# Kernel optimization log

Measured on AMD Instinct MI355X. Metric: run time of the kernel, lower is better.

Reference implementation:

```python
import jax, jax.numpy as jnp
import numpy as np

B, S, DM, H = 4, 1024, 1024, 16
DK = DM // H  # 64, must equal embeddim=64

def _linear(x, W, b):
    # torch nn.Linear: y = x @ W.T + b, W is [out, in]
    return jnp.matmul(x, W.T) + b

def setup_inputs() -> dict:
    key = jax.random.key(0)
    ks = jax.random.split(key, 40)
    inp = {}
    inp["query"] = jax.random.normal(ks[0], (B, S, DM), jnp.float32)
    inp["key"] = jax.random.normal(ks[1], (B, S, DM), jnp.float32)
    inp["value"] = jax.random.normal(ks[2], (B, S, DM), jnp.float32)
    inp["mask"] = jnp.ones((B, S, S), jnp.int32)
    def mk(i, dout, din):
        W = jax.random.normal(ks[i], (dout, din), jnp.float32) / np.sqrt(din).astype(np.float32)
        b = jax.random.normal(ks[i + 20], (dout,), jnp.float32) * 0.01
        return W, b
    # the 4 d_model x d_model projection linears (q, k, v, out)
    inp["Wq"], inp["bq"] = mk(3, DM, DM)
    inp["Wk"], inp["bk"] = mk(4, DM, DM)
    inp["Wv"], inp["bv"] = mk(5, DM, DM)
    inp["Wo"], inp["bo"] = mk(6, DM, DM)
    # the 64x64 refinement linears
    inp["Wkl"], inp["bkl"] = mk(7, DK, DK)   # key_linear
    inp["Wql"], inp["bql"] = mk(8, DK, DK)   # query_linear
    inp["Wq2"], inp["bq2"] = mk(9, DK, DK)   # query2_linear
    inp["Wvl"], inp["bvl"] = mk(10, DK, DK)  # value_linear
    inp["Wel"], inp["bel"] = mk(11, DK, DK)  # embed_linear
    return inp

def reference(query, key, value, mask,
              Wq, bq, Wk, bk, Wv, bv, Wo, bo,
              Wkl, bkl, Wql, bql, Wq2, bq2, Wvl, bvl, Wel, bel):
    b, s, dm = query.shape
    # project and split heads: [b, h, s, d_k]
    def split(x):
        return x.reshape(b, s, H, DK).transpose(0, 2, 1, 3)
    q = split(_linear(query, Wq, bq))
    k = split(_linear(key, Wk, bk))
    v = split(_linear(value, Wv, bv))
    # per-head 64x64 refinements with relu
    key_refine = jax.nn.relu(_linear(k, Wkl, bkl))
    q1 = jax.nn.relu(_linear(q, Wql, bql))
    q1 = jax.nn.relu(_linear(q1, Wel, bel))
    q2 = jax.nn.relu(_linear(q, Wq2, bq2))
    v_refine = jax.nn.relu(_linear(v, Wvl, bvl))
    # two attention-like matmuls (no 1/sqrt(d_k) scaling in original)
    qv = jnp.einsum("bhqd,bhkd->bhqk", q2, v_refine)
    kq = jnp.einsum("bhqd,bhkd->bhqk", q1, key_refine)
    m = mask[:, None, :, :]  # mask.unsqueeze(1)
    kq = jnp.where(m == 0, jnp.float32(-1e9), kq)
    attn = jax.nn.softmax(kq, axis=-1)
    # elementwise combine, then matmul against raw projected key (not value!)
    out = jnp.einsum("bhqk,bhkd->bhqd", attn * qv, k)
    out = out.transpose(0, 2, 1, 3).reshape(b, s, dm)
    return _linear(out, Wo, bo)
```

## Files before the change

kernel.cpp:

```cpp
#include <hip/hip_runtime.h>
#include <hip/hip_bf16.h>

#define B_  4
#define S_  1024
#define DM_ 1024
#define H_  16
#define DK_ 64

typedef unsigned short u16;
typedef __attribute__((ext_vector_type(8))) short bf16x8;
typedef __attribute__((ext_vector_type(4))) float f32x4;

__device__ __forceinline__ float bf2f(u16 u) {
    union { unsigned int i; float f; } c;
    c.i = ((unsigned int)u) << 16;
    return c.f;
}
__device__ __forceinline__ u16 f2bf(float f) {
    union { float f; unsigned int i; } c;
    c.f = f;
    unsigned int x = c.i;
    unsigned int lsb = (x >> 16) & 1u;
    x += 0x7fffu + lsb;
    return (u16)(x >> 16);
}
__device__ __forceinline__ u16 f2bf_fast(float f) {
    __hip_bfloat16 h = __float2bfloat16(f);
    return *reinterpret_cast<u16*>(&h);
}

__device__ __forceinline__ void async_ld16(const u16* g, u16* l) {
    __builtin_amdgcn_global_load_lds(
        (const __attribute__((address_space(1))) unsigned int*)(const void*)g,
        (__attribute__((address_space(3))) unsigned int*)(void*)l, 16, 0, 0);
}

__global__ void detect_kernel(const u16* __restrict__ q, int* __restrict__ flag) {
    int lane = threadIdx.x & 63;
    int cnt = 0;
#pragma unroll
    for (int i = 0; i < 4; ++i) {
        u16 u = q[2 * (lane * 4 + i)];
        int e = (u >> 7) & 0xFF;
        cnt += (e >= 100 && e <= 140) ? 1 : 0;
    }
#pragma unroll
    for (int off = 1; off < 64; off <<= 1) cnt += __shfl_xor(cnt, off, 64);
    if (lane == 0) *flag = (cnt < 128) ? 1 : 0;
}

#define NSEG 12
struct CvtArgs {
    const void* src[NSEG];
    void*       dst[NSEG];
    unsigned    off[NSEG + 1];
};

__global__ __launch_bounds__(256) void prep_kernel(
    CvtArgs a, unsigned total, const int* __restrict__ flag,
    const int* __restrict__ mask, int* __restrict__ tflags)
{
    const int tid = threadIdx.x;
    if (blockIdx.x < 512) {
        const int bx = blockIdx.x;
        const int kt = bx & 15, b = (bx >> 4) & 3, z = bx >> 6;
        int ok = 1;
#pragma unroll
        for (int i = tid; i < 128 * 16; i += 256) {
            int row = z * 128 + (i >> 4), seg = i & 15;
            int4 m = *(const int4*)&mask[((size_t)b * S_ + row) * S_ + kt * 64 + seg * 4];
            ok &= (m.x != 0) & (m.y != 0) & (m.z != 0) & (m.w != 0);
        }
        if (!ok) atomicOr(&tflags[b * 16 + kt], 1);
        return;
    }
    if (!*flag) return;
    unsigned v = (blockIdx.x - 512) * 256 + tid;
    if (v >= total) return;
    int s = 0;
    while (s < NSEG - 1 && v >= a.off[s + 1]) ++s;
    unsigned local = v - a.off[s];
    u16* dp = (u16*)a.dst[s] + (size_t)local * 8;
    const float* sp = (const float*)a.src[s] + (size_t)local * 8;
    float4 x = *(const float4*)sp, y = *(const float4*)(sp + 4);
    u16 t[8] = {f2bf(x.x), f2bf(x.y), f2bf(x.z), f2bf(x.w),
                f2bf(y.x), f2bf(y.y), f2bf(y.z), f2bf(y.w)};
    *(uint4*)dp = *(uint4*)t;
}

__global__ __launch_bounds__(256) void transpose_kernel(
    const u16* __restrict__ kp, u16* __restrict__ kpt)
{
    __shared__ u16 T[64][65];
    const int s0 = blockIdx.x * 64, h = blockIdx.y, b = blockIdx.z;
    const int tid = threadIdx.x;
    const size_t base = (size_t)b * S_ * DM_ + (size_t)h * DK_;
    for (int c = tid; c < 512; c += 256) {
        int row = c >> 3, cc = (c & 7) * 8;
        union { uint4 v; u16 u[8]; } x;
        x.v = *(const uint4*)&kp[base + (size_t)(s0 + row) * DM_ + cc];
#pragma unroll
        for (int j = 0; j < 8; ++j) T[row][cc + j] = x.u[j];
    }
    __syncthreads();
    const size_t baseT = (size_t)(b * H_ + h) * DK_ * S_;
    for (int c = tid; c < 512; c += 256) {
        int d = c >> 3, ss = (c & 7) * 8;
        u16 t[8];
#pragma unroll
        for (int j = 0; j < 8; ++j) t[j] = T[ss + j][d];
        *(uint4*)&kpt[baseT + (size_t)d * S_ + s0 + ss] = *(uint4*)t;
    }
}

struct QKVArgs {
    const u16* A0[3]; const u16* A1[3];
    const u16* W0[3]; const u16* W1[3];
    const void* bias[3];
    const u16* R10[3]; const u16* R11[3];
    const void* rb1[3];
    const u16* R20; const u16* R21; const void* rb2;
    const u16* R30; const u16* R31; const void* rb3;
    u16 *Kp, *q1b, *q2r, *krb, *vrb;
};

__global__ __launch_bounds__(256, 3) void qkv_fused_kernel(
    QKVArgs a, const int* __restrict__ flag)
{
    __shared__ __align__(16) u16 smem[16384];
    u16 (*As)[64] = (u16(*)[64])smem;
    u16 (*Ws)[64] = (u16(*)[64])(smem + 8192);

    const int z = blockIdx.z;
    const int f = *flag;
    const u16* __restrict__ A = f ? a.A1[z] : a.A0[z];
    const u16* __restrict__ W = f ? a.W1[z] : a.W0[z];
    const void* biasp = a.bias[z];

    const int m0   = blockIdx.y * 128;
    const int n0   = blockIdx.x * 128;
    const int tid  = threadIdx.x;
    const int w    = tid >> 6;
    const int lane = tid & 63;
    const int l16  = lane & 15;
    const int quad = lane >> 4;
    const int wr   = (w >> 1) * 64;
    const int wc   = (w & 1) * 64;

    const int srow = lane >> 3;
    const int sgrp = (lane & 7) ^ srow;

    f32x4 acc[4][4];
#pragma unroll
    for (int rt = 0; rt < 4; ++rt)
#pragma unroll
        for (int ct = 0; ct < 4; ++ct) acc[rt][ct] = (f32x4){0.f, 0.f, 0.f, 0.f};

    for (int k0 = 0; k0 < DM_; k0 += 64) {
#pragma unroll
        for (int s = 0; s < 4; ++s) {
            int seg = w * 4 + s;
            async_ld16(&A[(size_t)(m0 + seg * 8 + srow) * DM_ + k0 + sgrp * 8],
                       &As[seg * 8][0]);
            async_ld16(&W[(size_t)(n0 + seg * 8 + srow) * DM_ + k0 + sgrp * 8],
                       &Ws[seg * 8][0]);
        }
        __syncthreads();
#pragma unroll
        for (int kk = 0; kk < 2; ++kk) {
            const int p = (kk * 4 + quad) ^ (l16 & 7);
            bf16x8 av[4], bv[4];
#pragma unroll
            for (int rt = 0; rt < 4; ++rt)
                av[rt] = *(const bf16x8*)&As[wr + rt * 16 + l16][p * 8];
#pragma unroll
            for (int ct = 0; ct < 4; ++ct)
                bv[ct] = *(const bf16x8*)&Ws[wc + ct * 16 + l16][p * 8];
#pragma unroll
            for (int rt = 0; rt < 4; ++rt)
#pragma unroll
                for (int ct = 0; ct < 4; ++ct)
                    acc[rt][ct] = __builtin_amdgcn_mfma_f32_16x16x32_bf16(
                        av[rt], bv[ct], acc[rt][ct], 0, 0, 0);
        }
        __syncthreads();
    }

    const int hcol = n0 + wc;
    u16 (*Es)[64] = (u16(*)[64])(smem + w * 4096);

#pragma unroll
    for (int ct = 0; ct < 4; ++ct) {
        int col = hcol + ct * 16 + l16;
        float bv = f ? ((const float*)biasp)[col] : bf2f(((const u16*)biasp)[col]);
#pragma unroll
        for (int rt = 0; rt < 4; ++rt)
#pragma unroll
            for (int r = 0; r < 4; ++r) {
                int ml = rt * 16 + quad * 4 + r;
                int cl = ct * 16 + l16;
                u16 bb = f2bf(acc[rt][ct][r] + bv);
                if (z == 1) a.Kp[(size_t)(m0 + wr + ml) * DM_ + col] = bb;
                Es[ml][((((cl >> 3) ^ (ml & 7)) << 3) | (cl & 7))] = bb;
            }
    }

    bf16x8 af[4][2];
#pragma unroll
    for (int rt = 0; rt < 4; ++rt)
#pragma unroll
        for (int kk = 0; kk < 2; ++kk)
            af[rt][kk] = *(const bf16x8*)
                &Es[rt * 16 + l16][(((kk * 4 + quad) ^ (l16 & 7)) << 3)];

    const u16* R1 = f ? a.R11[z] : a.R10[z];
    bf16x8 wb[2][4];
#pragma unroll
    for (int kk = 0; kk < 2; ++kk)
#pragma unroll
        for (int ct = 0; ct < 4; ++ct)
            wb[kk][ct] = *(const bf16x8*)
                &R1[(size_t)(ct * 16 + l16) * 64 + kk * 32 + quad * 8];

    f32x4 r1[4][4];
#pragma unroll
    for (int rt = 0; rt < 4; ++rt)
#pragma unroll
        for (int ct = 0; ct < 4; ++ct) r1[rt][ct] = (f32x4){0.f, 0.f, 0.f, 0.f};
#pragma unroll
    for (int kk = 0; kk < 2; ++kk)
#pragma unroll
        for (int rt = 0; rt < 4; ++rt)
#pragma unroll
            for (int ct = 0; ct < 4; ++ct)
                r1[rt][ct] = __builtin_amdgcn_mfma_f32_16x16x32_bf16(
                    af[rt][kk], wb[kk][ct], r1[rt][ct], 0, 0, 0);

    if (z != 0) {
        const void* rb = a.rb1[z];
        u16* out = (z == 1) ? a.krb : a.vrb;
#pragma unroll
        for (int ct = 0; ct < 4; ++ct) {
            int cl = ct * 16 + l16;
            float bv = f ? ((const float*)rb)[cl] : bf2f(((const u16*)rb)[cl]);
#pragma unroll
            for (int rt = 0; rt < 4; ++rt)
#pragma unroll
                for (int r = 0; r < 4; ++r) {
                    float v = r1[rt][ct][r] + bv;
                    v = v > 0.f ? v : 0.f;
                    out[(size_t)(m0 + wr + rt * 16 + quad * 4 + r) * DM_ + hcol + cl]
                        = f2bf(v);
                }
        }
    } else {
        {
            const void* rb = a.rb1[0];
#pragma unroll
            for (int ct = 0; ct < 4; ++ct) {
                int cl = ct * 16 + l16;
                float bv = f ? ((const float*)rb)[cl] : bf2f(((const u16*)rb)[cl]);
#pragma unroll
                for (int rt = 0; rt < 4; ++rt)
#pragma unroll
                    for (int r = 0; r < 4; ++r) {
                        float v = r1[rt][ct][r] + bv;
                        v = v > 0.f ? v : 0.f;
                        int ml = rt * 16 + quad * 4 + r;
                        Es[ml][((((cl >> 3) ^ (ml & 7)) << 3) | (cl & 7))] = f2bf(v);
                    }
            }
        }
        {
            const u16* R3 = f ? a.R31 : a.R30;
#pragma unroll
            for (int kk = 0; kk < 2; ++kk)
#pragma unroll
                for (int ct = 0; ct < 4; ++ct)
                    wb[kk][ct] = *(const bf16x8*)
                        &R3[(size_t)(ct * 16 + l16) * 64 + kk * 32 + quad * 8];
            f32x4 r3[4][4];
#pragma unroll
            for (int rt = 0; rt < 4; ++rt)
#pragma unroll
                for (int ct = 0; ct < 4; ++ct) r3[rt][ct] = (f32x4){0.f, 0.f, 0.f, 0.f};
#pragma unroll
            for (int kk = 0; kk < 2; ++kk)
#pragma unroll
                for (int rt = 0; rt < 4; ++rt)
#pragma unroll
                    for (int ct = 0; ct < 4; ++ct)
                        r3[rt][ct] = __builtin_amdgcn_mfma_f32_16x16x32_bf16(
                            af[rt][kk], wb[kk][ct], r3[rt][ct], 0, 0, 0);
            const void* rb = a.rb3;
#pragma unroll
            for (int ct = 0; ct < 4; ++ct) {
                int cl = ct * 16 + l16;
                float bv = f ? ((const float*)rb)[cl] : bf2f(((const u16*)rb)[cl]);
#pragma unroll
                for (int rt = 0; rt < 4; ++rt)
#pragma unroll
                    for (int r = 0; r < 4; ++r) {
                        float v = r3[rt][ct][r] + bv;
                        v = v > 0.f ? v : 0.f;
                        a.q2r[(size_t)(m0 + wr + rt * 16 + quad * 4 + r) * DM_
                              + hcol + cl] = f2bf(v);
                    }
            }
        }
        {
#pragma unroll
            for (int rt = 0; rt < 4; ++rt)
#pragma unroll
                for (int kk = 0; kk < 2; ++kk)
                    af[rt][kk] = *(const bf16x8*)
                        &Es[rt * 16 + l16][(((kk * 4 + quad) ^ (l16 & 7)) << 3)];
            const u16* R2 = f ? a.R21 : a.R20;
#pragma unroll
            for (int kk = 0; kk < 2; ++kk)
#pragma unroll
                for (int ct = 0; ct < 4; ++ct)
                    wb[kk][ct] = *(const bf16x8*)
                        &R2[(size_t)(ct * 16 + l16) * 64 + kk * 32 + quad * 8];
            f32x4 r2[4][4];
#pragma unroll
            for (int rt = 0; rt < 4; ++rt)
#pragma unroll
                for (int ct = 0; ct < 4; ++ct) r2[rt][ct] = (f32x4){0.f, 0.f, 0.f, 0.f};
#pragma unroll
            for (int kk = 0; kk < 2; ++kk)
#pragma unroll
                for (int rt = 0; rt < 4; ++rt)
#pragma unroll
                    for (int ct = 0; ct < 4; ++ct)
                        r2[rt][ct] = __builtin_amdgcn_mfma_f32_16x16x32_bf16(
                            af[rt][kk], wb[kk][ct], r2[rt][ct], 0, 0, 0);
            const void* rb = a.rb2;
#pragma unroll
            for (int ct = 0; ct < 4; ++ct) {
                int cl = ct * 16 + l16;
                float bv = f ? ((const float*)rb)[cl] : bf2f(((const u16*)rb)[cl]);
#pragma unroll
                for (int rt = 0; rt < 4; ++rt)
#pragma unroll
                    for (int r = 0; r < 4; ++r) {
                        float v = r2[rt][ct][r] + bv;
                        v = v > 0.f ? v : 0.f;
                        a.q1b[(size_t)(m0 + wr + rt * 16 + quad * 4 + r) * DM_
                              + hcol + cl] = f2bf(v);
                    }
            }
        }
    }
}

__global__ __launch_bounds__(256, 3) void gemm_async_kernel(
    const u16* __restrict__ Ain, const u16* __restrict__ W0,
    const u16* __restrict__ W1, const void* __restrict__ biasp,
    void* __restrict__ Cp, const int* __restrict__ flag)
{
    __shared__ __align__(16) u16 As[128][64];
    __shared__ __align__(16) u16 Ws[128][64];

    const int f = *flag;
    const u16* __restrict__ W = f ? W1 : W0;

    const int m0   = blockIdx.y * 128;
    const int n0   = blockIdx.x * 128;
    const int tid  = threadIdx.x;
    const int w    = tid >> 6;
    const int lane = tid & 63;
    const int l16  = lane & 15;
    const int quad = lane >> 4;
    const int wr   = (w >> 1) * 64;
    const int wc   = (w & 1) * 64;

    const int srow = lane >> 3;
    const int sgrp = (lane & 7) ^ srow;

    f32x4 acc[4][4];
#pragma unroll
    for (int rt = 0; rt < 4; ++rt)
#pragma unroll
        for (int ct = 0; ct < 4; ++ct) acc[rt][ct] = (f32x4){0.f, 0.f, 0.f, 0.f};

    for (int k0 = 0; k0 < DM_; k0 += 64) {
#pragma unroll
        for (int s = 0; s < 4; ++s) {
            int seg = w * 4 + s;
            async_ld16(&Ain[(size_t)(m0 + seg * 8 + srow) * DM_ + k0 + sgrp * 8],
                       &As[seg * 8][0]);
            async_ld16(&W[(size_t)(n0 + seg * 8 + srow) * DM_ + k0 + sgrp * 8],
                       &Ws[seg * 8][0]);
        }
        __syncthreads();
#pragma unroll
        for (int kk = 0; kk < 2; ++kk) {
            const int p = (kk * 4 + quad) ^ (l16 & 7);
            bf16x8 av[4], bv[4];
#pragma unroll
            for (int rt = 0; rt < 4; ++rt)
                av[rt] = *(const bf16x8*)&As[wr + rt * 16 + l16][p * 8];
#pragma unroll
            for (int ct = 0; ct < 4; ++ct)
                bv[ct] = *(const bf16x8*)&Ws[wc + ct * 16 + l16][p * 8];
#pragma unroll
            for (int rt = 0; rt < 4; ++rt)
#pragma unroll
                for (int ct = 0; ct < 4; ++ct)
                    acc[rt][ct] = __builtin_amdgcn_mfma_f32_16x16x32_bf16(
                        av[rt], bv[ct], acc[rt][ct], 0, 0, 0);
        }
        __syncthreads();
    }

#pragma unroll
    for (int ct = 0; ct < 4; ++ct) {
        int col = n0 + wc + ct * 16 + l16;
        float bv = f ? ((const float*)biasp)[col] : bf2f(((const u16*)biasp)[col]);
#pragma unroll
        for (int rt = 0; rt < 4; ++rt)
#pragma unroll
            for (int r = 0; r < 4; ++r) {
                int row = m0 + wr + rt * 16 + quad * 4 + r;
                float v = acc[rt][ct][r] + bv;
                size_t idx = (size_t)row * DM_ + col;
                if (f) ((float*)Cp)[idx] = v;
                else   ((u16*)Cp)[idx]   = f2bf(v);
            }
    }
}

__global__ __launch_bounds__(256, 2) void attn_kernel(
    const u16* __restrict__ q1, const u16* __restrict__ q2,
    const u16* __restrict__ kr, const u16* __restrict__ vr,
    const u16* __restrict__ kpt, const int* __restrict__ mask,
    const int* __restrict__ tflags, u16* __restrict__ om)
{
    __shared__ __align__(16) u16 krs[2][64][64];
    __shared__ __align__(16) u16 vrs[2][64][64];
    __shared__ __align__(16) u16 kts[2][64][64];
    __shared__ __align__(16) u16 pts[4][32][72];

    const int bid  = blockIdx.x;
    const int orig = (bid & 7) * 64 + (bid >> 3);
    const int qt = orig & 7;
    const int h  = (orig >> 3) & 15;
    const int b  = orig >> 7;

    const int q0   = qt * 128;
    const int tid  = threadIdx.x;
    const int w    = tid >> 6;
    const int lane = tid & 63;
    const int l16  = lane & 15;
    const int quad = lane >> 4;

    const size_t base  = (size_t)b * S_ * DM_ + (size_t)h * DK_;
    const size_t baseT = (size_t)(b * H_ + h) * DK_ * S_;

    const int srow = lane >> 3;
    const int sgrp = (lane & 7) ^ srow;

#define STAGE_TILES(buf, kn)                                                   \
    {                                                                          \
        _Pragma("unroll")                                                      \
        for (int i = 0; i < 6; ++i) {                                          \
            int s_ = w * 6 + i;                                                \
            int t_ = s_ >> 3;                                                  \
            int r8 = (s_ & 7) * 8;                                             \
            if (t_ == 0)                                                       \
                async_ld16(&kr[base + (size_t)((kn) + r8 + srow) * DM_ +       \
                               sgrp * 8], &krs[buf][r8][0]);                   \
            else if (t_ == 1)                                                  \
                async_ld16(&vr[base + (size_t)((kn) + r8 + srow) * DM_ +       \
                               sgrp * 8], &vrs[buf][r8][0]);                   \
            else                                                               \
                async_ld16(&kpt[baseT + (size_t)(r8 + srow) * S_ + (kn) +      \
                                sgrp * 8], &kts[buf][r8][0]);                  \
        }                                                                      \
    }

    bf16x8 a1[2][2], a2[2][2];
#pragma unroll
    for (int rt = 0; rt < 2; ++rt) {
        const int qrow = q0 + w * 32 + rt * 16 + l16;
#pragma unroll
        for (int kk = 0; kk < 2; ++kk) {
            a1[rt][kk] = *(const bf16x8*)&q1[base + (size_t)qrow * DM_ + kk * 32 + quad * 8];
            a2[rt][kk] = *(const bf16x8*)&q2[base + (size_t)qrow * DM_ + kk * 32 + quad * 8];
        }
    }

    float m_run[2][4], l_run[2][4];
    f32x4 oacc[2][4];
#pragma unroll
    for (int rt = 0; rt < 2; ++rt)
#pragma unroll
        for (int r = 0; r < 4; ++r) { m_run[rt][r] = -1e30f; l_run[rt][r] = 0.f; }
#pragma unroll
    for (int rt = 0; rt < 2; ++rt)
#pragma unroll
        for (int ct = 0; ct < 4; ++ct) oacc[rt][ct] = (f32x4){0.f, 0.f, 0.f, 0.f};

    STAGE_TILES(0, 0)
    __syncthreads();

    for (int kt = 0; kt < S_ / 64; ++kt) {
        const int cur = kt & 1;
        const int k0  = kt * 64;
        const bool pf = (kt + 1 < S_ / 64);

        if (pf) STAGE_TILES(cur ^ 1, k0 + 64)

        const int tf = tflags[b * 16 + kt];

        f32x4 s1[2][4], s2[2][4];
#pragma unroll
        for (int rt = 0; rt < 2; ++rt)
#pragma unroll
            for (int ct = 0; ct < 4; ++ct) {
                s1[rt][ct] = (f32x4){0.f, 0.f, 0.f, 0.f};
                s2[rt][ct] = (f32x4){0.f, 0.f, 0.f, 0.f};
            }
        __builtin_amdgcn_s_setprio(1);
#pragma unroll
        for (int kk = 0; kk < 2; ++kk) {
            const int p = ((kk * 4 + quad) ^ (l16 & 7)) * 8;
            bf16x8 b1[4], b2[4];
#pragma unroll
            for (int ct = 0; ct < 4; ++ct) {
                b1[ct] = *(const bf16x8*)&krs[cur][ct * 16 + l16][p];
                b2[ct] = *(const bf16x8*)&vrs[cur][ct * 16 + l16][p];
            }
#pragma unroll
            for (int rt = 0; rt < 2; ++rt)
#pragma unroll
                for (int ct = 0; ct < 4; ++ct) {
                    s1[rt][ct] = __builtin_amdgcn_mfma_f32_16x16x32_bf16(
                        a1[rt][kk], b1[ct], s1[rt][ct], 0, 0, 0);
                    s2[rt][ct] = __builtin_amdgcn_mfma_f32_16x16x32_bf16(
                        a2[rt][kk], b2[ct], s2[rt][ct], 0, 0, 0);
                }
        }
        __builtin_amdgcn_s_setprio(0);

        if (tf) {
#pragma unroll
            for (int rt = 0; rt < 2; ++rt)
#pragma unroll
                for (int ct = 0; ct < 4; ++ct)
#pragma unroll
                    for (int r = 0; r < 4; ++r) {
                        int qrow = q0 + w * 32 + rt * 16 + quad * 4 + r;
                        int kc   = k0 + ct * 16 + l16;
                        if (mask[((size_t)b * S_ + qrow) * S_ + kc] == 0)
                            s1[rt][ct][r] = -1e9f;
                    }
        }

        float tmax[2][4];
#pragma unroll
        for (int rt = 0; rt < 2; ++rt)
#pragma unroll
            for (int r = 0; r < 4; ++r) tmax[rt][r] = -1e30f;
#pragma unroll
        for (int rt = 0; rt < 2; ++rt)
#pragma unroll
            for (int ct = 0; ct < 4; ++ct)
#pragma unroll
                for (int r = 0; r < 4; ++r)
                    tmax[rt][r] = fmaxf(tmax[rt][r], s1[rt][ct][r]);
#pragma unroll
        for (int off = 1; off < 16; off <<= 1)
#pragma unroll
            for (int rt = 0; rt < 2; ++rt)
#pragma unroll
                for (int r = 0; r < 4; ++r)
                    tmax[rt][r] = fmaxf(tmax[rt][r], __shfl_xor(tmax[rt][r], off, 64));

        float alpha[2][4], newm[2][4];
#pragma unroll
        for (int rt = 0; rt < 2; ++rt)
#pragma unroll
            for (int r = 0; r < 4; ++r) {
                newm[rt][r]  = fmaxf(m_run[rt][r], tmax[rt][r]);
                alpha[rt][r] = __expf(m_run[rt][r] - newm[rt][r]);
                m_run[rt][r] = newm[rt][r];
            }

        float psum[2][4] = {};
#pragma unroll
        for (int rt = 0; rt < 2; ++rt)
#pragma unroll
            for (int ct = 0; ct < 4; ++ct)
#pragma unroll
                for (int r = 0; r < 4; ++r) {
                    float p = __expf(s1[rt][ct][r] - newm[rt][r]);
                    psum[rt][r] += p;
                    pts[w][rt * 16 + quad * 4 + r][ct * 16 + l16] =
                        f2bf_fast(p * s2[rt][ct][r]);
                }
#pragma unroll
        for (int off = 1; off < 16; off <<= 1)
#pragma unroll
            for (int rt = 0; rt < 2; ++rt)
#pragma unroll
                for (int r = 0; r < 4; ++r)
                    psum[rt][r] += __shfl_xor(psum[rt][r], off, 64);
#pragma unroll
        for (int rt = 0; rt < 2; ++rt)
#pragma unroll
            for (int r = 0; r < 4; ++r)
                l_run[rt][r] = l_run[rt][r] * alpha[rt][r] + psum[rt][r];
#pragma unroll
        for (int rt = 0; rt < 2; ++rt)
#pragma unroll
            for (int ct = 0; ct < 4; ++ct)
#pragma unroll
                for (int r = 0; r < 4; ++r) oacc[rt][ct][r] *= alpha[rt][r];

        {
            __builtin_amdgcn_s_setprio(1);
            bf16x8 bb[2][4];
#pragma unroll
            for (int kk = 0; kk < 2; ++kk) {
                const int p = ((kk * 4 + quad) ^ (l16 & 7)) * 8;
#pragma unroll
                for (int ct = 0; ct < 4; ++ct)
                    bb[kk][ct] = *(const bf16x8*)&kts[cur][ct * 16 + l16][p];
            }
#pragma unroll
            for (int rt = 0; rt < 2; ++rt)
#pragma unroll
                for (int kk = 0; kk < 2; ++kk) {
                    bf16x8 a = *(const bf16x8*)&pts[w][rt * 16 + l16][kk * 32 + quad * 8];
#pragma unroll
                    for (int ct = 0; ct < 4; ++ct)
                        oacc[rt][ct] = __builtin_amdgcn_mfma_f32_16x16x32_bf16(
                            a, bb[kk][ct], oacc[rt][ct], 0, 0, 0);
                }
            __builtin_amdgcn_s_setprio(0);
        }

        if (pf) __syncthreads();
    }

#pragma unroll
    for (int rt = 0; rt < 2; ++rt)
#pragma unroll
        for (int ct = 0; ct < 4; ++ct)
#pragma unroll
            for (int r = 0; r < 4; ++r) {
                int row = q0 + w * 32 + rt * 16 + quad * 4 + r;
                int col = ct * 16 + l16;
                float v = oacc[rt][ct][r] / l_run[rt][r];
                om[base + (size_t)row * DM_ + col] = f2bf_fast(v);
            }
#undef STAGE_TILES
}

extern "C" void kernel_launch(void* const* d_in, const int* in_sizes, int n_in,
                              void* d_out, int out_size, void* d_ws, size_t ws_size,
                              hipStream_t stream)
{
    const void* query = d_in[0];
    const void* key   = d_in[1];
    const void* value = d_in[2];
    const int*  mask  = (const int*)d_in[3];
    const void* Wq  = d_in[4];  const void* bq  = d_in[5];
    const void* Wk  = d_in[6];  const void* bk  = d_in[7];
    const void* Wv  = d_in[8];  const void* bv  = d_in[9];
    const void* Wo  = d_in[10]; const void* bo  = d_in[11];
    const void* Wkl = d_in[12]; const void* bkl = d_in[13];
    const void* Wql = d_in[14]; const void* bql = d_in[15];
    const void* Wq2 = d_in[16]; const void* bq2 = d_in[17];
    const void* Wvl = d_in[18]; const void* bvl = d_in[19];
    const void* Wel = d_in[20]; const void* bel = d_in[21];

    int* flag   = (int*)d_ws;
    int* tflags = (int*)d_ws + 4;
    u16* ws     = (u16*)((char*)d_ws + 512);
    const size_t BUF = (size_t)(B_ * S_) * DM_;
    u16* Kp  = ws + 0 * BUF;
    u16* krb = ws + 1 * BUF;
    u16* q1b = ws + 2 * BUF;
    u16* q2r = ws + 3 * BUF;
    u16* vrb = ws + 4 * BUF;
    u16* Om  = ws + 5 * BUF;
    u16* KpT = ws + 6 * BUF;
    u16* Qc  = ws + 7 * BUF;
    u16* Kc  = ws + 8 * BUF;
    u16* Vc  = ws + 9 * BUF;
    u16* Wbig = ws + 10 * BUF;
    u16* Wqc = Wbig + 0 * (size_t)(DM_ * DM_);
    u16* Wkc = Wbig + 1 * (size_t)(DM_ * DM_);
    u16* Wvc = Wbig + 2 * (size_t)(DM_ * DM_);
    u16* Woc = Wbig + 3 * (size_t)(DM_ * DM_);
    u16* Wsm = Wbig + 4 * (size_t)(DM_ * DM_);
    u16* Wklc = Wsm + 0 * (DK_ * DK_);
    u16* Wqlc = Wsm + 1 * (DK_ * DK_);
    u16* Welc = Wsm + 2 * (DK_ * DK_);
    u16* Wq2c = Wsm + 3 * (DK_ * DK_);
    u16* Wvlc = Wsm + 4 * (DK_ * DK_);

    const int M = B_ * S_;
    dim3 blk(256);

    detect_kernel<<<1, 64, 0, stream>>>((const u16*)query, flag);

    hipMemsetAsync(tflags, 0, 64 * sizeof(int), stream);
    CvtArgs ca;
    const unsigned VIN = (unsigned)(BUF / 8);
    const unsigned VWB = (unsigned)(DM_ * DM_ / 8);
    const unsigned VWS = (unsigned)(DK_ * DK_ / 8);
    const void* srcs[NSEG] = {query, key, value, Wq, Wk, Wv, Wo, Wkl, Wql, Wel, Wq2, Wvl};
    void* dsts[NSEG] = {Qc, Kc, Vc, Wqc, Wkc, Wvc, Woc, Wklc, Wqlc, Welc, Wq2c, Wvlc};
    unsigned vcn[NSEG] = {VIN, VIN, VIN, VWB, VWB, VWB, VWB, VWS, VWS, VWS, VWS, VWS};
    unsigned off = 0;
    for (int i = 0; i < NSEG; ++i) { ca.src[i] = srcs[i]; ca.dst[i] = dsts[i]; ca.off[i] = off; off += vcn[i]; }
    ca.off[NSEG] = off;
    prep_kernel<<<dim3(512 + (off + 255) / 256), blk, 0, stream>>>(ca, off, flag, mask, tflags);

    QKVArgs qa = {};
    qa.A0[0] = (const u16*)query; qa.A1[0] = Qc;
    qa.A0[1] = (const u16*)key;   qa.A1[1] = Kc;
    qa.A0[2] = (const u16*)value; qa.A1[2] = Vc;
    qa.W0[0] = (const u16*)Wq; qa.W1[0] = Wqc;
    qa.W0[1] = (const u16*)Wk; qa.W1[1] = Wkc;
    qa.W0[2] = (const u16*)Wv; qa.W1[2] = Wvc;
    qa.bias[0] = bq; qa.bias[1] = bk; qa.bias[2] = bv;
    qa.R10[0] = (const u16*)Wql; qa.R11[0] = Wqlc; qa.rb1[0] = bql;
    qa.R10[1] = (const u16*)Wkl; qa.R11[1] = Wklc; qa.rb1[1] = bkl;
    qa.R10[2] = (const u16*)Wvl; qa.R11[2] = Wvlc; qa.rb1[2] = bvl;
    qa.R20 = (const u16*)Wel; qa.R21 = Welc; qa.rb2 = bel;
    qa.R30 = (const u16*)Wq2; qa.R31 = Wq2c; qa.rb3 = bq2;
    qa.Kp = Kp; qa.q1b = q1b; qa.q2r = q2r; qa.krb = krb; qa.vrb = vrb;
    dim3 gBig(DM_ / 128, M / 128, 3);
    qkv_fused_kernel<<<gBig, blk, 0, stream>>>(qa, flag);

    dim3 gT(S_ / 64, H_, B_);
    transpose_kernel<<<gT, blk, 0, stream>>>(Kp, KpT);

    attn_kernel<<<dim3(512), blk, 0, stream>>>(q1b, q2r, krb, vrb, KpT, mask, tflags, Om);

    dim3 gO(DM_ / 128, M / 128);
    gemm_async_kernel<<<gO, blk, 0, stream>>>(Om, (const u16*)Wo, Woc, bo, d_out, flag);
}
```

Before: 309.9 us.

## Compute transposed score tiles so softmax reductions stay in-lane

Swaps the MFMA operand order so each lane holds one query row across several key columns, which means the row max and row sum need only two cross-lane shuffles instead of four per value. The running max and sum become one scalar per query tile, and probability products are written to LDS as packed pairs of bf16. The alpha and final normalisation are broadcast back to the output accumulator layout with __shfl, and the divide becomes a reciprocal multiply. This adds extra shuffles for the rescale and makes the mask reads less coalesced.

After: 290.0 us. 6.4% less time.

```diff
diff --git a/kernel.cpp b/kernel.cpp
--- a/kernel.cpp
+++ b/kernel.cpp
@@ -491,12 +491,10 @@
         }
     }
 
-    float m_run[2][4], l_run[2][4];
+    float m_run[2], l_run[2];
     f32x4 oacc[2][4];
 #pragma unroll
-    for (int rt = 0; rt < 2; ++rt)
-#pragma unroll
-        for (int r = 0; r < 4; ++r) { m_run[rt][r] = -1e30f; l_run[rt][r] = 0.f; }
+    for (int qt2 = 0; qt2 < 2; ++qt2) { m_run[qt2] = -1e30f; l_run[qt2] = 0.f; }
 #pragma unroll
     for (int rt = 0; rt < 2; ++rt)
 #pragma unroll
@@ -514,13 +512,13 @@
 
         const int tf = tflags[b * 16 + kt];
 
-        f32x4 s1[2][4], s2[2][4];
-#pragma unroll
-        for (int rt = 0; rt < 2; ++rt)
-#pragma unroll
-            for (int ct = 0; ct < 4; ++ct) {
-                s1[rt][ct] = (f32x4){0.f, 0.f, 0.f, 0.f};
-                s2[rt][ct] = (f32x4){0.f, 0.f, 0.f, 0.f};
+        f32x4 st1[2][4], st2[2][4];
+#pragma unroll
+        for (int qt2 = 0; qt2 < 2; ++qt2)
+#pragma unroll
+            for (int kt4 = 0; kt4 < 4; ++kt4) {
+                st1[qt2][kt4] = (f32x4){0.f, 0.f, 0.f, 0.f};
+                st2[qt2][kt4] = (f32x4){0.f, 0.f, 0.f, 0.f};
             }
         __builtin_amdgcn_s_setprio(1);
 #pragma unroll
@@ -528,96 +526,79 @@
             const int p = ((kk * 4 + quad) ^ (l16 & 7)) * 8;
             bf16x8 b1[4], b2[4];
 #pragma unroll
-            for (int ct = 0; ct < 4; ++ct) {
-                b1[ct] = *(const bf16x8*)&krs[cur][ct * 16 + l16][p];
-                b2[ct] = *(const bf16x8*)&vrs[cur][ct * 16 + l16][p];
-            }
-#pragma unroll
-            for (int rt = 0; rt < 2; ++rt)
-#pragma unroll
-                for (int ct = 0; ct < 4; ++ct) {
-                    s1[rt][ct] = __builtin_amdgcn_mfma_f32_16x16x32_bf16(
-                        a1[rt][kk], b1[ct], s1[rt][ct], 0, 0, 0);
-                    s2[rt][ct] = __builtin_amdgcn_mfma_f32_16x16x32_bf16(
-                        a2[rt][kk], b2[ct], s2[rt][ct], 0, 0, 0);
+            for (int kt4 = 0; kt4 < 4; ++kt4) {
+                b1[kt4] = *(const bf16x8*)&krs[cur][kt4 * 16 + l16][p];
+                b2[kt4] = *(const bf16x8*)&vrs[cur][kt4 * 16 + l16][p];
+            }
+#pragma unroll
+            for (int qt2 = 0; qt2 < 2; ++qt2)
+#pragma unroll
+                for (int kt4 = 0; kt4 < 4; ++kt4) {
+                    st1[qt2][kt4] = __builtin_amdgcn_mfma_f32_16x16x32_bf16(
+                        b1[kt4], a1[qt2][kk], st1[qt2][kt4], 0, 0, 0);
+                    st2[qt2][kt4] = __builtin_amdgcn_mfma_f32_16x16x32_bf16(
+                        b2[kt4], a2[qt2][kk], st2[qt2][kt4], 0, 0, 0);
                 }
         }
         __builtin_amdgcn_s_setprio(0);
 
         if (tf) {
 #pragma unroll
-            for (int rt = 0; rt < 2; ++rt)
-#pragma unroll
-                for (int ct = 0; ct < 4; ++ct)
+            for (int qt2 = 0; qt2 < 2; ++qt2)
+#pragma unroll
+                for (int kt4 = 0; kt4 < 4; ++kt4)
 #pragma unroll
                     for (int r = 0; r < 4; ++r) {
-                        int qrow = q0 + w * 32 + rt * 16 + quad * 4 + r;
-                        int kc   = k0 + ct * 16 + l16;
+                        int qrow = q0 + w * 32 + qt2 * 16 + l16;
+                        int kc   = k0 + kt4 * 16 + quad * 4 + r;
                         if (mask[((size_t)b * S_ + qrow) * S_ + kc] == 0)
-                            s1[rt][ct][r] = -1e9f;
+                            st1[qt2][kt4][r] = -1e9f;
                     }
         }
 
-        float tmax[2][4];
+        float alphaq[2], newm[2];
+#pragma unroll
+        for (int qt2 = 0; qt2 < 2; ++qt2) {
+            float m = st1[qt2][0][0];
+#pragma unroll
+            for (int kt4 = 0; kt4 < 4; ++kt4)
+#pragma unroll
+                for (int r = 0; r < 4; ++r)
+                    m = fmaxf(m, st1[qt2][kt4][r]);
+            m = fmaxf(m, __shfl_xor(m, 16, 64));
+            m = fmaxf(m, __shfl_xor(m, 32, 64));
+            newm[qt2]   = fmaxf(m_run[qt2], m);
+            alphaq[qt2] = __expf(m_run[qt2] - newm[qt2]);
+            m_run[qt2]  = newm[qt2];
+        }
+
+#pragma unroll
+        for (int qt2 = 0; qt2 < 2; ++qt2) {
+            float s = 0.f;
+#pragma unroll
+            for (int kt4 = 0; kt4 < 4; ++kt4)
+#pragma unroll
+                for (int pp = 0; pp < 2; ++pp) {
+                    float p0 = __expf(st1[qt2][kt4][2 * pp]     - newm[qt2]);
+                    float p1 = __expf(st1[qt2][kt4][2 * pp + 1] - newm[qt2]);
+                    s += p0 + p1;
+                    unsigned u = (unsigned)f2bf_fast(p0 * st2[qt2][kt4][2 * pp])
+                               | ((unsigned)f2bf_fast(p1 * st2[qt2][kt4][2 * pp + 1]) << 16);
+                    *(unsigned*)&pts[w][qt2 * 16 + l16][kt4 * 16 + quad * 4 + 2 * pp] = u;
+                }
+            s += __shfl_xor(s, 16, 64);
+            s += __shfl_xor(s, 32, 64);
+            l_run[qt2] = l_run[qt2] * alphaq[qt2] + s;
+        }
+
 #pragma unroll
         for (int rt = 0; rt < 2; ++rt)
 #pragma unroll
-            for (int r = 0; r < 4; ++r) tmax[rt][r] = -1e30f;
-#pragma unroll
-        for (int rt = 0; rt < 2; ++rt)
-#pragma unroll
-            for (int ct = 0; ct < 4; ++ct)
-#pragma unroll
-                for (int r = 0; r < 4; ++r)
-                    tmax[rt][r] = fmaxf(tmax[rt][r], s1[rt][ct][r]);
-#pragma unroll
-        for (int off = 1; off < 16; off <<= 1)
-#pragma unroll
-            for (int rt = 0; rt < 2; ++rt)
-#pragma unroll
-                for (int r = 0; r < 4; ++r)
-                    tmax[rt][r] = fmaxf(tmax[rt][r], __shfl_xor(tmax[rt][r], off, 64));
-
-        float alpha[2][4], newm[2][4];
-#pragma unroll
-        for (int rt = 0; rt < 2; ++rt)
-#pragma unroll
             for (int r = 0; r < 4; ++r) {
-                newm[rt][r]  = fmaxf(m_run[rt][r], tmax[rt][r]);
-                alpha[rt][r] = __expf(m_run[rt][r] - newm[rt][r]);
-                m_run[rt][r] = newm[rt][r];
-            }
-
-        float psum[2][4] = {};
-#pragma unroll
-        for (int rt = 0; rt < 2; ++rt)
-#pragma unroll
-            for (int ct = 0; ct < 4; ++ct)
-#pragma unroll
-                for (int r = 0; r < 4; ++r) {
-                    float p = __expf(s1[rt][ct][r] - newm[rt][r]);
-                    psum[rt][r] += p;
-                    pts[w][rt * 16 + quad * 4 + r][ct * 16 + l16] =
-                        f2bf_fast(p * s2[rt][ct][r]);
-                }
-#pragma unroll
-        for (int off = 1; off < 16; off <<= 1)
-#pragma unroll
-            for (int rt = 0; rt < 2; ++rt)
-#pragma unroll
-                for (int r = 0; r < 4; ++r)
-                    psum[rt][r] += __shfl_xor(psum[rt][r], off, 64);
-#pragma unroll
-        for (int rt = 0; rt < 2; ++rt)
-#pragma unroll
-            for (int r = 0; r < 4; ++r)
-                l_run[rt][r] = l_run[rt][r] * alpha[rt][r] + psum[rt][r];
-#pragma unroll
-        for (int rt = 0; rt < 2; ++rt)
-#pragma unroll
-            for (int ct = 0; ct < 4; ++ct)
-#pragma unroll
-                for (int r = 0; r < 4; ++r) oacc[rt][ct][r] *= alpha[rt][r];
+                float ao = __shfl(alphaq[rt], quad * 4 + r, 64);
+#pragma unroll
+                for (int ct = 0; ct < 4; ++ct) oacc[rt][ct][r] *= ao;
+            }
 
         {
             __builtin_amdgcn_s_setprio(1);
@@ -648,14 +629,16 @@
 #pragma unroll
     for (int rt = 0; rt < 2; ++rt)
 #pragma unroll
-        for (int ct = 0; ct < 4; ++ct)
-#pragma unroll
-            for (int r = 0; r < 4; ++r) {
+        for (int r = 0; r < 4; ++r) {
+            float lo = __shfl(l_run[rt], quad * 4 + r, 64);
+            float inv = 1.f / lo;
+#pragma unroll
+            for (int ct = 0; ct < 4; ++ct) {
                 int row = q0 + w * 32 + rt * 16 + quad * 4 + r;
                 int col = ct * 16 + l16;
-                float v = oacc[rt][ct][r] / l_run[rt][r];
-                om[base + (size_t)row * DM_ + col] = f2bf_fast(v);
-            }
+                om[base + (size_t)row * DM_ + col] = f2bf_fast(oacc[rt][ct][r] * inv);
+            }
+        }
 #undef STAGE_TILES
 }
 
```
